# Kernel tuning notes

Measured on AMD Instinct MI355X. Metric: run time of the kernel, lower is better.

The kernel has to match this reference:

```python
import jax, jax.numpy as jnp
import numpy as np

B, S, K_DIM = 2, 2048, 2048
H, H_KV = 32, 8
HD = K_DIM // H  # 64
THETA = 10000.0


def apply_rope(x, position_ids, theta):
    # x: (B, H, S, hd), position_ids: (B, S) -- interleaved (even/odd) RoPE
    hd = x.shape[-1]
    dtype = x.dtype
    inv_freq = 1.0 / theta ** (jnp.arange(0, hd, 2, dtype=dtype) / hd)  # (hd/2,)
    freqs = position_ids.astype(dtype)[:, :, None] * inv_freq           # (B, S, hd/2)
    sin = jnp.sin(freqs)[:, None]  # (B, 1, S, hd/2)
    cos = jnp.cos(freqs)[:, None]
    x1 = x[..., ::2]
    x2 = x[..., 1::2]
    even = x1 * cos - x2 * sin
    odd = x2 * cos + x1 * sin
    return jnp.stack([even, odd], axis=-1).reshape(x.shape)


def setup_inputs() -> dict:
    key = jax.random.key(0)
    ks = jax.random.split(key, 5)
    x = jax.random.normal(ks[0], (B, S, K_DIM), dtype=jnp.float32)
    position_ids = jnp.broadcast_to(jnp.arange(S, dtype=jnp.int32)[None, :], (B, S))
    attention_mask = jnp.ones((B, S), dtype=jnp.int32)
    scale = 0.02
    Wq = jax.random.normal(ks[1], (H * HD, K_DIM), dtype=jnp.float32) * scale
    Wk = jax.random.normal(ks[2], (H_KV * HD, K_DIM), dtype=jnp.float32) * scale
    Wv = jax.random.normal(ks[3], (H_KV * HD, K_DIM), dtype=jnp.float32) * scale
    Wo = jax.random.normal(ks[4], (K_DIM, K_DIM), dtype=jnp.float32) * scale
    return {"x": x, "position_ids": position_ids, "attention_mask": attention_mask,
            "Wq": Wq, "Wk": Wk, "Wv": Wv, "Wo": Wo}


def reference(x, position_ids, attention_mask, Wq, Wk, Wv, Wo):
    b, s, kd = x.shape
    hd = HD
    q = (x @ Wq.T).reshape(b, s, H, hd).transpose(0, 2, 1, 3)     # (B, H, S, hd)
    k = (x @ Wk.T).reshape(b, s, H_KV, hd).transpose(0, 2, 1, 3)  # (B, Hkv, S, hd)
    v = (x @ Wv.T).reshape(b, s, H_KV, hd).transpose(0, 2, 1, 3)
    q = apply_rope(q, position_ids, THETA)
    k = apply_rope(k, position_ids, THETA)
    rep = H // H_KV
    # repeat_interleave over head dim == expand-within-group then flatten
    k = jnp.broadcast_to(k[:, :, None], (b, H_KV, rep, s, hd)).reshape(b, H, s, hd)
    v = jnp.broadcast_to(v[:, :, None], (b, H_KV, rep, s, hd)).reshape(b, H, s, hd)
    causal = jnp.triu(jnp.ones((s, s), dtype=bool), 1)            # True = masked
    pad = (attention_mask == 0)[:, None, None, :]                 # (B,1,1,S)
    mask = causal[None, None, :, :] | pad                         # (B,1,S,S) -> broadcast over H
    scores = jnp.einsum('bhqd,bhkd->bhqk', q, k) / jnp.sqrt(jnp.asarray(hd, x.dtype))
    scores = jnp.where(mask, jnp.finfo(scores.dtype).min, scores)
    attn = jax.nn.softmax(scores, axis=-1)
    out = jnp.einsum('bhqk,bhkd->bhqd', attn, v)
    out = out.transpose(0, 2, 1, 3).reshape(b, s, kd)
    return out @ Wo.T
```

## Files before the change

### kernel.cpp

```cpp
#include <hip/hip_runtime.h>
#include <hip/hip_bf16.h>

#define S_LEN 2048
#define BATCH 2
#define KDIM  2048
#define NH    32
#define NKV   8
#define HDIM  64

typedef short bf16s;
typedef short bf16x8 __attribute__((ext_vector_type(8)));
typedef short bf16x4 __attribute__((ext_vector_type(4)));
typedef float f32x4  __attribute__((ext_vector_type(4)));

#define KSCALE 0.1803368801111f

__device__ __forceinline__ bf16s f2bf(float f) {
  __hip_bfloat16 h = __float2bfloat16(f);
  return *reinterpret_cast<bf16s*>(&h);
}
__device__ __forceinline__ float ex2(float x) { return __builtin_amdgcn_exp2f(x); }

__device__ __forceinline__ void gload16(const void* g, void* l) {
  __builtin_amdgcn_global_load_lds(
      (const __attribute__((address_space(1))) char*)g,
      (__attribute__((address_space(3))) char*)l, 16, 0, 0);
}

__global__ void k_cvt_all(const float* __restrict__ s0, const float* __restrict__ s1,
                          const float* __restrict__ s2, const float* __restrict__ s3,
                          const float* __restrict__ s4, bf16s* __restrict__ dst,
                          float* __restrict__ qtab, float* __restrict__ ktab,
                          const int* __restrict__ pos) {
  const int t = blockIdx.x * blockDim.x + threadIdx.x;
  if (t < S_LEN * 32) {
    const int p = t >> 5, i = t & 31;
    const float inv = expf(-(float)(2 * i) * (1.0f / 64.0f) * 9.210340371976184f);
    const float fr = (float)p * inv;
    const float c = cosf(fr), s = sinf(fr);
    ktab[2 * t]     = c;
    ktab[2 * t + 1] = s;
    qtab[2 * t]     = c * KSCALE;
    qtab[2 * t + 1] = s * KSCALE;
  }
  const int NU = 2359296;
  const int stride = gridDim.x * blockDim.x;
  for (int u = t; u < NU; u += stride) {
    const int e = u * 8;
    const float* src; int off;
    if (e < 8388608)       { src = s0; off = e; }
    else if (e < 12582912) { src = s1; off = e - 8388608; }
    else if (e < 13631488) { src = s2; off = e - 12582912; }
    else if (e < 14680064) { src = s3; off = e - 13631488; }
    else                   { src = s4; off = e - 14680064; }
    float4 a = *(const float4*)(src + off);
    float4 b = *(const float4*)(src + off + 4);
    bf16x8 o;
    o[0]=f2bf(a.x); o[1]=f2bf(a.y); o[2]=f2bf(a.z); o[3]=f2bf(a.w);
    o[4]=f2bf(b.x); o[5]=f2bf(b.y); o[6]=f2bf(b.z); o[7]=f2bf(b.w);
    *(bf16x8*)(dst + e) = o;
  }
}

__global__ __launch_bounds__(256, 2)
void k_gemm_qkv(const bf16s* __restrict__ A, const bf16s* __restrict__ Bw,
                const int* __restrict__ pos,
                const float* __restrict__ qtab, const float* __restrict__ ktab,
                bf16s* __restrict__ qb, bf16s* __restrict__ kb, bf16s* __restrict__ vtb) {
  const int K = KDIM;
  __shared__ bf16s As[128 * 64];
  __shared__ bf16s Bs[128 * 64];
  const int tid  = threadIdx.x;
  const int lane = tid & 63;
  const int w    = tid >> 6;
  const int wr   = w >> 1, wc = w & 1;
  const int l15  = lane & 15, lg = lane >> 4;
  const int h0 = blockIdx.y * 24 + blockIdx.x;
  const int sw = (h0 & 7) * 96 + (h0 >> 3);
  const int bx = sw % 24;
  const int by = sw / 24;

  f32x4 acc[4][4] = {};

  const int srow = (w << 3) + (lane >> 3);
  const int sc8  = ((lane & 7) ^ (lane >> 3)) << 3;
  const bf16s* gA = A  + (size_t)(by * 128 + srow) * K + sc8;
  const bf16s* gB = Bw + (size_t)(bx * 128 + srow) * K + sc8;
  bf16s* lA = &As[(w << 3) * 64];
  bf16s* lB = &Bs[(w << 3) * 64];

  const int nkt = K >> 6;
  for (int kt = 0; kt < nkt; ++kt) {
    __syncthreads();
    const int ko = kt << 6;
#pragma unroll
    for (int j = 0; j < 4; ++j) {
      gload16(gA + (size_t)(j * 32) * K + ko, lA + j * 2048);
      gload16(gB + (size_t)(j * 32) * K + ko, lB + j * 2048);
    }
    __syncthreads();

#pragma unroll
    for (int kk = 0; kk < 2; ++kk) {
      bf16x8 av[4], bv[4];
#pragma unroll
      for (int i = 0; i < 4; ++i) {
        const int ra = wr * 64 + i * 16 + l15;
        av[i] = *(const bf16x8*)&As[ra * 64 + ((kk * 32 + lg * 8) ^ ((ra & 7) << 3))];
        const int rb = wc * 64 + i * 16 + l15;
        bv[i] = *(const bf16x8*)&Bs[rb * 64 + ((kk * 32 + lg * 8) ^ ((rb & 7) << 3))];
      }
#pragma unroll
      for (int mi = 0; mi < 4; ++mi)
#pragma unroll
        for (int ni = 0; ni < 4; ++ni)
          acc[mi][ni] = __builtin_amdgcn_mfma_f32_16x16x32_bf16(av[mi], bv[ni], acc[mi][ni], 0, 0, 0);
    }
  }

#pragma unroll
  for (int mi = 0; mi < 4; ++mi) {
    const int m0 = by * 128 + wr * 64 + mi * 16 + 4 * lg;
#pragma unroll
    for (int ni = 0; ni < 4; ++ni) {
      const int n = bx * 128 + wc * 64 + ni * 16 + l15;
      if (bx < 16) {
        const int d = n & 63, i = d >> 1;
        const float sgn = (d & 1) ? 1.f : -1.f;
#pragma unroll
        for (int r = 0; r < 4; ++r) {
          const int m = m0 + r;
          const float val = acc[mi][ni][r];
          const float par = __shfl_xor(val, 1);
          const float2 cs = *(const float2*)&qtab[((size_t)pos[m] << 6) + (i << 1)];
          qb[(size_t)m * KDIM + n] = f2bf(val * cs.x + sgn * par * cs.y);
        }
      } else if (bx < 20) {
        const int col = n - 2048;
        const int d = col & 63, i = d >> 1;
        const float sgn = (d & 1) ? 1.f : -1.f;
#pragma unroll
        for (int r = 0; r < 4; ++r) {
          const int m = m0 + r;
          const float val = acc[mi][ni][r];
          const float par = __shfl_xor(val, 1);
          const float2 cs = *(const float2*)&ktab[((size_t)pos[m] << 6) + (i << 1)];
          kb[(size_t)m * 512 + col] = f2bf(val * cs.x + sgn * par * cs.y);
        }
      } else {
        const int col = n - 2560;
        const int kvh = col >> 6, d = col & 63;
        const int b = m0 >> 11, s = m0 & (S_LEN - 1);
        bf16x4 pk;
#pragma unroll
        for (int r = 0; r < 4; ++r) pk[r] = f2bf(acc[mi][ni][r]);
        *(bf16x4*)&vtb[((size_t)((b * NKV + kvh) * HDIM + d)) * S_LEN + s] = pk;
      }
    }
  }
}

__global__ __launch_bounds__(256, 2)
void k_gemm_o(const bf16s* __restrict__ A, const bf16s* __restrict__ Bw,
              float* __restrict__ C, int N, int K) {
  __shared__ bf16s As[128 * 64];
  __shared__ bf16s Bs[128 * 64];
  const int tid  = threadIdx.x;
  const int lane = tid & 63;
  const int w    = tid >> 6;
  const int wr   = w >> 1, wc = w & 1;
  const int l15  = lane & 15, lg = lane >> 4;
  const int h0 = blockIdx.y * 16 + blockIdx.x;
  const int sw = (h0 & 7) * 64 + (h0 >> 3);
  const int bx = sw & 15;
  const int by = sw >> 4;

  f32x4 acc[4][4] = {};

  const int srow = (w << 3) + (lane >> 3);
  const int sc8  = ((lane & 7) ^ (lane >> 3)) << 3;
  const bf16s* gA = A  + (size_t)(by * 128 + srow) * K + sc8;
  const bf16s* gB = Bw + (size_t)(bx * 128 + srow) * K + sc8;
  bf16s* lA = &As[(w << 3) * 64];
  bf16s* lB = &Bs[(w << 3) * 64];

  const int nkt = K >> 6;
  for (int kt = 0; kt < nkt; ++kt) {
    __syncthreads();
    const int ko = kt << 6;
#pragma unroll
    for (int j = 0; j < 4; ++j) {
      gload16(gA + (size_t)(j * 32) * K + ko, lA + j * 2048);
      gload16(gB + (size_t)(j * 32) * K + ko, lB + j * 2048);
    }
    __syncthreads();

#pragma unroll
    for (int kk = 0; kk < 2; ++kk) {
      bf16x8 av[4], bv[4];
#pragma unroll
      for (int i = 0; i < 4; ++i) {
        const int ra = wr * 64 + i * 16 + l15;
        av[i] = *(const bf16x8*)&As[ra * 64 + ((kk * 32 + lg * 8) ^ ((ra & 7) << 3))];
        const int rb = wc * 64 + i * 16 + l15;
        bv[i] = *(const bf16x8*)&Bs[rb * 64 + ((kk * 32 + lg * 8) ^ ((rb & 7) << 3))];
      }
#pragma unroll
      for (int mi = 0; mi < 4; ++mi)
#pragma unroll
        for (int ni = 0; ni < 4; ++ni)
          acc[mi][ni] = __builtin_amdgcn_mfma_f32_16x16x32_bf16(av[mi], bv[ni], acc[mi][ni], 0, 0, 0);
    }
  }

#pragma unroll
  for (int mi = 0; mi < 4; ++mi) {
    const int m0 = by * 128 + wr * 64 + mi * 16 + 4 * lg;
#pragma unroll
    for (int ni = 0; ni < 4; ++ni) {
      const int n = bx * 128 + wc * 64 + ni * 16 + l15;
#pragma unroll
      for (int r = 0; r < 4; ++r)
        C[(size_t)(m0 + r) * N + n] = acc[mi][ni][r];
    }
  }
}

__global__ __launch_bounds__(256, 3)
void k_flash(const bf16s* __restrict__ q, const bf16s* __restrict__ k,
             const bf16s* __restrict__ vt, const int* __restrict__ amask,
             bf16s* __restrict__ out) {
  __shared__ bf16s Ks[2][64 * 64];
  __shared__ bf16s Vs[2][64 * 64];
  __shared__ bf16s Ps[4][32 * 64];

  const int tid = threadIdx.x, lane = tid & 63, w = tid >> 6;
  const int l15 = lane & 15, lg = lane >> 4;
  const int bh = blockIdx.x;
  const int y = blockIdx.y, yq = y & 3, hi = (y >> 3) & 1;
  const int qt = (y & 4) ? (yq + (hi << 2)) : ((hi ? 11 : 15) - yq);
  const int b = bh >> 5, h = bh & 31, kvh = h >> 2;
  const int nt = 2 * qt + 2;

  bf16x8 aq[2][2];
  const int qbase = qt * 128 + w * 32;
#pragma unroll
  for (int u = 0; u < 2; ++u) {
    const size_t qr = (size_t)(b * S_LEN + qbase + u * 16 + l15);
#pragma unroll
    for (int s = 0; s < 2; ++s)
      aq[u][s] = *(const bf16x8*)(q + qr * KDIM + h * HDIM + s * 32 + lg * 8);
  }

  const bf16s* kbase = k + (size_t)b * S_LEN * (NKV * HDIM) + kvh * HDIM;
  const bf16s* vbase = vt + ((size_t)(b * NKV + kvh) * HDIM) * S_LEN;

  const int srow0 = w * 16 + (lane >> 3);
  const int scol0 = (lane & 7) ^ (srow0 & 7);
  const int srow1 = srow0 + 8;
  const int scol1 = (lane & 7) ^ (srow1 & 7);

  auto stage = [&](int kt, int bufi) {
    gload16(kbase + (size_t)(kt * 64 + srow0) * (NKV * HDIM) + scol0 * 8, &Ks[bufi][w * 1024]);
    gload16(kbase + (size_t)(kt * 64 + srow1) * (NKV * HDIM) + scol1 * 8, &Ks[bufi][w * 1024 + 512]);
    gload16(vbase + (size_t)srow0 * S_LEN + kt * 64 + scol0 * 8, &Vs[bufi][w * 1024]);
    gload16(vbase + (size_t)srow1 * S_LEN + kt * 64 + scol1 * 8, &Vs[bufi][w * 1024 + 512]);
  };

  float m_run[2] = {-1e30f, -1e30f}, l_run[2] = {0.f, 0.f};
  f32x4 ao[2][4] = {};

  stage(0, 0);
  __syncthreads();

  int buf = 0;
  for (int kt = 0; kt < nt; ++kt) {
    if (kt + 1 < nt) stage(kt + 1, buf ^ 1);

    const unsigned long long bm = __ballot(amask[b * S_LEN + kt * 64 + lane] != 0);
    const bool allok = (bm == ~0ull);
    const bool diag = (kt >= nt - 2);

    f32x4 sc[2][4] = {};
    __builtin_amdgcn_s_setprio(1);
#pragma unroll
    for (int c = 0; c < 4; ++c) {
      const int row = c * 16 + l15;
      const bf16s* kp = &Ks[buf][row * 64];
      const int xw = (row & 7) << 3;
      bf16x8 kb0 = *(const bf16x8*)(kp + ((lg * 8) ^ xw));
      bf16x8 kb1 = *(const bf16x8*)(kp + ((32 + lg * 8) ^ xw));
      sc[0][c] = __builtin_amdgcn_mfma_f32_16x16x32_bf16(kb0, aq[0][0], sc[0][c], 0, 0, 0);
      sc[0][c] = __builtin_amdgcn_mfma_f32_16x16x32_bf16(kb1, aq[0][1], sc[0][c], 0, 0, 0);
      sc[1][c] = __builtin_amdgcn_mfma_f32_16x16x32_bf16(kb0, aq[1][0], sc[1][c], 0, 0, 0);
      sc[1][c] = __builtin_amdgcn_mfma_f32_16x16x32_bf16(kb1, aq[1][1], sc[1][c], 0, 0, 0);
    }
    __builtin_amdgcn_s_setprio(0);

#pragma unroll
    for (int u = 0; u < 2; ++u) {
      const int qg = qt * 128 + w * 32 + u * 16 + l15;
      float mt = -1e30f;
      if (diag || !allok) {
#pragma unroll
        for (int c = 0; c < 4; ++c)
#pragma unroll
          for (int r = 0; r < 4; ++r) {
            const int kg = kt * 64 + c * 16 + lg * 4 + r;
            float s = sc[u][c][r];
            if ((kg > qg) || (!allok && !((bm >> (kg & 63)) & 1))) s = -1e30f;
            sc[u][c][r] = s;
            mt = fmaxf(mt, s);
          }
      } else {
#pragma unroll
        for (int c = 0; c < 4; ++c)
#pragma unroll
          for (int r = 0; r < 4; ++r) mt = fmaxf(mt, sc[u][c][r]);
      }
      mt = fmaxf(mt, __shfl_xor(mt, 16));
      mt = fmaxf(mt, __shfl_xor(mt, 32));
      if (!__all(mt <= m_run[u])) {
        const float mn = fmaxf(m_run[u], mt);
        const float al = ex2(m_run[u] - mn);
        m_run[u] = mn;
        l_run[u] *= al;
#pragma unroll
        for (int vc = 0; vc < 4; ++vc)
#pragma unroll
          for (int r = 0; r < 4; ++r) ao[u][vc][r] *= al;
      }
      const float mb = m_run[u];
      float ls = 0.f;
#pragma unroll
      for (int c = 0; c < 4; ++c) {
        bf16x4 pk;
#pragma unroll
        for (int r = 0; r < 4; ++r) {
          const float p = ex2(sc[u][c][r] - mb);
          ls += p;
          pk[r] = f2bf(p);
        }
        const int prow = u * 16 + l15;
        *(bf16x4*)&Ps[w][prow * 64 + ((c * 16 + lg * 4) ^ ((prow & 7) << 3))] = pk;
      }
      ls += __shfl_xor(ls, 16);
      ls += __shfl_xor(ls, 32);
      l_run[u] += ls;
    }

    bf16x8 pa[2][2];
#pragma unroll
    for (int u = 0; u < 2; ++u) {
      const int prow = u * 16 + l15;
      const int px = (prow & 7) << 3;
#pragma unroll
      for (int s = 0; s < 2; ++s)
        pa[u][s] = *(const bf16x8*)&Ps[w][prow * 64 + ((s * 32 + lg * 8) ^ px)];
    }

    __builtin_amdgcn_s_setprio(1);
#pragma unroll
    for (int vc = 0; vc < 4; ++vc) {
      const int row = vc * 16 + l15;
      const bf16s* vp = &Vs[buf][row * 64];
      const int xw = (row & 7) << 3;
      bf16x8 vb0 = *(const bf16x8*)(vp + ((lg * 8) ^ xw));
      bf16x8 vb1 = *(const bf16x8*)(vp + ((32 + lg * 8) ^ xw));
      ao[0][vc] = __builtin_amdgcn_mfma_f32_16x16x32_bf16(vb0, pa[0][0], ao[0][vc], 0, 0, 0);
      ao[0][vc] = __builtin_amdgcn_mfma_f32_16x16x32_bf16(vb1, pa[0][1], ao[0][vc], 0, 0, 0);
      ao[1][vc] = __builtin_amdgcn_mfma_f32_16x16x32_bf16(vb0, pa[1][0], ao[1][vc], 0, 0, 0);
      ao[1][vc] = __builtin_amdgcn_mfma_f32_16x16x32_bf16(vb1, pa[1][1], ao[1][vc], 0, 0, 0);
    }
    __builtin_amdgcn_s_setprio(0);

    __syncthreads();
    buf ^= 1;
  }

#pragma unroll
  for (int u = 0; u < 2; ++u) {
    const float inv = 1.0f / l_run[u];
    const size_t m = (size_t)b * S_LEN + qt * 128 + w * 32 + u * 16 + l15;
#pragma unroll
    for (int vc = 0; vc < 4; ++vc) {
      bf16x4 ov;
#pragma unroll
      for (int r = 0; r < 4; ++r) ov[r] = f2bf(ao[u][vc][r] * inv);
      *(bf16x4*)&out[m * KDIM + h * HDIM + vc * 16 + lg * 4] = ov;
    }
  }
}

extern "C" void kernel_launch(void* const* d_in, const int* in_sizes, int n_in,
                              void* d_out, int out_size, void* d_ws, size_t ws_size,
                              hipStream_t stream) {
  const float* x  = (const float*)d_in[0];
  const int* pos  = (const int*)d_in[1];
  const int* am   = (const int*)d_in[2];
  const float* Wq = (const float*)d_in[3];
  const float* Wk = (const float*)d_in[4];
  const float* Wv = (const float*)d_in[5];
  const float* Wo = (const float*)d_in[6];
  float* out = (float*)d_out;

  char* ws = (char*)d_ws;
  const int M = BATCH * S_LEN;
  bf16s* xb   = (bf16s*)(ws);
  bf16s* wqkv = (bf16s*)(ws + 16777216);
  bf16s* wob  = (bf16s*)(ws + 29360128);
  bf16s* qb   = (bf16s*)(ws + 37748736);
  bf16s* kb   = (bf16s*)(ws + 54525952);
  bf16s* vtb  = (bf16s*)(ws + 58720256);
  bf16s* aob  = (bf16s*)(ws + 62914560);
  float* qtab = (float*)(ws + 62914560);
  float* ktab = (float*)(ws + 63438848);

  dim3 blk(256);

  k_cvt_all<<<dim3(2048), blk, 0, stream>>>(x, Wq, Wk, Wv, Wo, xb, qtab, ktab, pos);

  k_gemm_qkv<<<dim3(24, 32), blk, 0, stream>>>(xb, wqkv, pos, qtab, ktab, qb, kb, vtb);

  k_flash<<<dim3(BATCH * NH, S_LEN / 128), blk, 0, stream>>>(qb, kb, vtb, am, aob);

  k_gemm_o<<<dim3(16, 32), blk, 0, stream>>>(aob, wob, out, 2048, 2048);
}
```

Measured before the change: 187.9 us.

## Widen flash-attention KV tiles to 128 keys per iteration

```diff
diff --git a/kernel.cpp b/kernel.cpp
--- a/kernel.cpp
+++ b/kernel.cpp
@@ -226,12 +226,12 @@
   }
 }
 
-__global__ __launch_bounds__(256, 3)
+__global__ __launch_bounds__(256, 2)
 void k_flash(const bf16s* __restrict__ q, const bf16s* __restrict__ k,
              const bf16s* __restrict__ vt, const int* __restrict__ amask,
              bf16s* __restrict__ out) {
-  __shared__ bf16s Ks[2][64 * 64];
-  __shared__ bf16s Vs[2][64 * 64];
+  __shared__ bf16s Ks[2][128 * 64];
+  __shared__ bf16s Vs[2][64 * 128];
   __shared__ bf16s Ps[4][32 * 64];
 
   const int tid = threadIdx.x, lane = tid & 63, w = tid >> 6;
@@ -240,7 +240,7 @@
   const int y = blockIdx.y, yq = y & 3, hi = (y >> 3) & 1;
   const int qt = (y & 4) ? (yq + (hi << 2)) : ((hi ? 11 : 15) - yq);
   const int b = bh >> 5, h = bh & 31, kvh = h >> 2;
-  const int nt = 2 * qt + 2;
+  const int nt = qt + 1;
 
   bf16x8 aq[2][2];
   const int qbase = qt * 128 + w * 32;
@@ -255,16 +255,16 @@
   const bf16s* kbase = k + (size_t)b * S_LEN * (NKV * HDIM) + kvh * HDIM;
   const bf16s* vbase = vt + ((size_t)(b * NKV + kvh) * HDIM) * S_LEN;
 
-  const int srow0 = w * 16 + (lane >> 3);
-  const int scol0 = (lane & 7) ^ (srow0 & 7);
-  const int srow1 = srow0 + 8;
-  const int scol1 = (lane & 7) ^ (srow1 & 7);
-
-  auto stage = [&](int kt, int bufi) {
-    gload16(kbase + (size_t)(kt * 64 + srow0) * (NKV * HDIM) + scol0 * 8, &Ks[bufi][w * 1024]);
-    gload16(kbase + (size_t)(kt * 64 + srow1) * (NKV * HDIM) + scol1 * 8, &Ks[bufi][w * 1024 + 512]);
-    gload16(vbase + (size_t)srow0 * S_LEN + kt * 64 + scol0 * 8, &Vs[bufi][w * 1024]);
-    gload16(vbase + (size_t)srow1 * S_LEN + kt * 64 + scol1 * 8, &Vs[bufi][w * 1024 + 512]);
+  auto stage = [&](int mt, int bufi) {
+#pragma unroll
+    for (int c = 0; c < 4; ++c) {
+      const int rK = w * 32 + 8 * c + (lane >> 3);
+      gload16(kbase + (size_t)(mt * 128 + rK) * (NKV * HDIM) + (((lane & 7) ^ (lane >> 3)) << 3),
+              &Ks[bufi][w * 2048 + c * 512]);
+      const int rV = w * 16 + 4 * c + (lane >> 4);
+      gload16(vbase + (size_t)rV * S_LEN + mt * 128 + (((lane & 15) ^ (rV & 7)) << 3),
+              &Vs[bufi][w * 2048 + c * 512]);
+    }
   };
 
   float m_run[2] = {-1e30f, -1e30f}, l_run[2] = {0.f, 0.f};
@@ -274,54 +274,58 @@
   __syncthreads();
 
   int buf = 0;
-  for (int kt = 0; kt < nt; ++kt) {
-    if (kt + 1 < nt) stage(kt + 1, buf ^ 1);
-
-    const unsigned long long bm = __ballot(amask[b * S_LEN + kt * 64 + lane] != 0);
-    const bool allok = (bm == ~0ull);
-    const bool diag = (kt >= nt - 2);
-
-    f32x4 sc[2][4] = {};
+  for (int mt = 0; mt < nt; ++mt) {
+    if (mt + 1 < nt) stage(mt + 1, buf ^ 1);
+
+    const unsigned long long bm0 = __ballot(amask[b * S_LEN + mt * 128 + lane] != 0);
+    const unsigned long long bm1 = __ballot(amask[b * S_LEN + mt * 128 + 64 + lane] != 0);
+    const bool allok = (bm0 == ~0ull) && (bm1 == ~0ull);
+    const bool diag = (mt == nt - 1);
+
+    f32x4 sc[2][8];
     __builtin_amdgcn_s_setprio(1);
 #pragma unroll
-    for (int c = 0; c < 4; ++c) {
+    for (int c = 0; c < 8; ++c) {
       const int row = c * 16 + l15;
       const bf16s* kp = &Ks[buf][row * 64];
       const int xw = (row & 7) << 3;
       bf16x8 kb0 = *(const bf16x8*)(kp + ((lg * 8) ^ xw));
       bf16x8 kb1 = *(const bf16x8*)(kp + ((32 + lg * 8) ^ xw));
-      sc[0][c] = __builtin_amdgcn_mfma_f32_16x16x32_bf16(kb0, aq[0][0], sc[0][c], 0, 0, 0);
+      f32x4 z = {};
+      sc[0][c] = __builtin_amdgcn_mfma_f32_16x16x32_bf16(kb0, aq[0][0], z, 0, 0, 0);
       sc[0][c] = __builtin_amdgcn_mfma_f32_16x16x32_bf16(kb1, aq[0][1], sc[0][c], 0, 0, 0);
-      sc[1][c] = __builtin_amdgcn_mfma_f32_16x16x32_bf16(kb0, aq[1][0], sc[1][c], 0, 0, 0);
+      sc[1][c] = __builtin_amdgcn_mfma_f32_16x16x32_bf16(kb0, aq[1][0], z, 0, 0, 0);
       sc[1][c] = __builtin_amdgcn_mfma_f32_16x16x32_bf16(kb1, aq[1][1], sc[1][c], 0, 0, 0);
     }
     __builtin_amdgcn_s_setprio(0);
 
+    float mb[2], ls[2] = {0.f, 0.f};
 #pragma unroll
     for (int u = 0; u < 2; ++u) {
       const int qg = qt * 128 + w * 32 + u * 16 + l15;
-      float mt = -1e30f;
+      float mt_ = -1e30f;
       if (diag || !allok) {
 #pragma unroll
-        for (int c = 0; c < 4; ++c)
+        for (int c = 0; c < 8; ++c)
 #pragma unroll
           for (int r = 0; r < 4; ++r) {
-            const int kg = kt * 64 + c * 16 + lg * 4 + r;
+            const int kg = mt * 128 + c * 16 + lg * 4 + r;
+            const unsigned long long bmv = (kg & 64) ? bm1 : bm0;
             float s = sc[u][c][r];
-            if ((kg > qg) || (!allok && !((bm >> (kg & 63)) & 1))) s = -1e30f;
+            if ((kg > qg) || (!allok && !((bmv >> (kg & 63)) & 1))) s = -1e30f;
             sc[u][c][r] = s;
-            mt = fmaxf(mt, s);
+            mt_ = fmaxf(mt_, s);
           }
       } else {
 #pragma unroll
-        for (int c = 0; c < 4; ++c)
-#pragma unroll
-          for (int r = 0; r < 4; ++r) mt = fmaxf(mt, sc[u][c][r]);
-      }
-      mt = fmaxf(mt, __shfl_xor(mt, 16));
-      mt = fmaxf(mt, __shfl_xor(mt, 32));
-      if (!__all(mt <= m_run[u])) {
-        const float mn = fmaxf(m_run[u], mt);
+        for (int c = 0; c < 8; ++c)
+#pragma unroll
+          for (int r = 0; r < 4; ++r) mt_ = fmaxf(mt_, sc[u][c][r]);
+      }
+      mt_ = fmaxf(mt_, __shfl_xor(mt_, 16));
+      mt_ = fmaxf(mt_, __shfl_xor(mt_, 32));
+      if (!__all(mt_ <= m_run[u])) {
+        const float mn = fmaxf(m_run[u], mt_);
         const float al = ex2(m_run[u] - mn);
         m_run[u] = mn;
         l_run[u] *= al;
@@ -330,49 +334,55 @@
 #pragma unroll
           for (int r = 0; r < 4; ++r) ao[u][vc][r] *= al;
       }
-      const float mb = m_run[u];
-      float ls = 0.f;
-#pragma unroll
-      for (int c = 0; c < 4; ++c) {
-        bf16x4 pk;
-#pragma unroll
-        for (int r = 0; r < 4; ++r) {
-          const float p = ex2(sc[u][c][r] - mb);
-          ls += p;
-          pk[r] = f2bf(p);
+      mb[u] = m_run[u];
+    }
+
+#pragma unroll
+    for (int hf = 0; hf < 2; ++hf) {
+      bf16x8 pa[2][2];
+#pragma unroll
+      for (int u = 0; u < 2; ++u) {
+        const int prow = u * 16 + l15;
+        const int pxw = (prow & 7) << 3;
+#pragma unroll
+        for (int c = 0; c < 4; ++c) {
+          const int cc = hf * 4 + c;
+          bf16x4 pk;
+#pragma unroll
+          for (int r = 0; r < 4; ++r) {
+            const float p = ex2(sc[u][cc][r] - mb[u]);
+            ls[u] += p;
+            pk[r] = f2bf(p);
+          }
+          *(bf16x4*)&Ps[w][prow * 64 + ((c * 16 + lg * 4) ^ pxw)] = pk;
         }
-        const int prow = u * 16 + l15;
-        *(bf16x4*)&Ps[w][prow * 64 + ((c * 16 + lg * 4) ^ ((prow & 7) << 3))] = pk;
-      }
-      ls += __shfl_xor(ls, 16);
-      ls += __shfl_xor(ls, 32);
-      l_run[u] += ls;
-    }
-
-    bf16x8 pa[2][2];
+        pa[u][0] = *(const bf16x8*)&Ps[w][prow * 64 + ((lg * 8) ^ pxw)];
+        pa[u][1] = *(const bf16x8*)&Ps[w][prow * 64 + ((32 + lg * 8) ^ pxw)];
+      }
+
+      __builtin_amdgcn_s_setprio(1);
+#pragma unroll
+      for (int vc = 0; vc < 4; ++vc) {
+        const int row = vc * 16 + l15;
+        const bf16s* vp = &Vs[buf][row * 128];
+        const int r7 = row & 7;
+#pragma unroll
+        for (int s = 0; s < 2; ++s) {
+          const bf16x8 vb = *(const bf16x8*)(vp + (((hf * 8 + s * 4 + lg) ^ r7) << 3));
+          ao[0][vc] = __builtin_amdgcn_mfma_f32_16x16x32_bf16(vb, pa[0][s], ao[0][vc], 0, 0, 0);
+          ao[1][vc] = __builtin_amdgcn_mfma_f32_16x16x32_bf16(vb, pa[1][s], ao[1][vc], 0, 0, 0);
+        }
+      }
+      __builtin_amdgcn_s_setprio(0);
+    }
+
 #pragma unroll
     for (int u = 0; u < 2; ++u) {
-      const int prow = u * 16 + l15;
-      const int px = (prow & 7) << 3;
-#pragma unroll
-      for (int s = 0; s < 2; ++s)
-        pa[u][s] = *(const bf16x8*)&Ps[w][prow * 64 + ((s * 32 + lg * 8) ^ px)];
-    }
-
-    __builtin_amdgcn_s_setprio(1);
-#pragma unroll
-    for (int vc = 0; vc < 4; ++vc) {
-      const int row = vc * 16 + l15;
-      const bf16s* vp = &Vs[buf][row * 64];
-      const int xw = (row & 7) << 3;
-      bf16x8 vb0 = *(const bf16x8*)(vp + ((lg * 8) ^ xw));
-      bf16x8 vb1 = *(const bf16x8*)(vp + ((32 + lg * 8) ^ xw));
-      ao[0][vc] = __builtin_amdgcn_mfma_f32_16x16x32_bf16(vb0, pa[0][0], ao[0][vc], 0, 0, 0);
-      ao[0][vc] = __builtin_amdgcn_mfma_f32_16x16x32_bf16(vb1, pa[0][1], ao[0][vc], 0, 0, 0);
-      ao[1][vc] = __builtin_amdgcn_mfma_f32_16x16x32_bf16(vb0, pa[1][0], ao[1][vc], 0, 0, 0);
-      ao[1][vc] = __builtin_amdgcn_mfma_f32_16x16x32_bf16(vb1, pa[1][1], ao[1][vc], 0, 0, 0);
-    }
-    __builtin_amdgcn_s_setprio(0);
+      float v = ls[u];
+      v += __shfl_xor(v, 16);
+      v += __shfl_xor(v, 32);
+      l_run[u] += v;
+    }
 
     __syncthreads();
     buf ^= 1;
```

Measured after the change: 197.2 us. 5.0% more time.
